# Performance work log

Hardware: AMD Instinct MI355X
Metric: run time of the kernel (lower is better)

The kernel has to match this reference:

```python
import jax, jax.numpy as jnp
import numpy as np

N = 20000      # num_nodes
H = 150        # hidden_channels
R = 35         # num_relations
B = 5          # num_blocks  -> block dims 30x30
E = 640000     # num_edges
IB = H // B


def _xavier(key, shape):
    fan_in, fan_out = shape[-2], shape[-1]
    lim = jnp.sqrt(6.0 / (fan_in + fan_out))
    return jax.random.uniform(key, shape, jnp.float32, -lim, lim)


def setup_inputs() -> dict:
    key = jax.random.key(0)
    ks = jax.random.split(key, 10)
    edge_index = jax.random.randint(ks[0], (2, E), 0, N, dtype=jnp.int64)
    edge_type = jax.random.randint(ks[1], (E,), 0, R, dtype=jnp.int64)
    return {
        "node_emb": _xavier(ks[2], (N, H)),
        "w1": _xavier(ks[3], (R, B, IB, IB)),      # relation block-diagonal weights
        "root1": _xavier(ks[4], (H, H)),
        "b1": jnp.zeros((H,), jnp.float32),
        "w2": _xavier(ks[5], (R, B, IB, IB)),
        "root2": _xavier(ks[6], (H, H)),
        "b2": jnp.zeros((H,), jnp.float32),
        "edge_index": edge_index,
        "edge_type": edge_type,
    }


def _rgcn_layer(x, w, root, bias, src, dst, etype):
    # PyG RGCNConv with num_blocks: per-relation block-diag transform of source
    # features, mean-aggregated per (dst, relation), summed over relations,
    # plus dense root transform and bias.
    # Linearity lets us aggregate (mean) FIRST, then transform: cheaper + exact.
    seg = dst * R + etype                                   # [E] segment per (node, rel)
    xs = x[src]                                             # [E, H] gather
    sums = jax.ops.segment_sum(xs, seg, num_segments=N * R)  # [N*R, H]
    cnt = jax.ops.segment_sum(jnp.ones((src.shape[0],), x.dtype), seg,
                              num_segments=N * R)           # [N*R]
    mean = sums / jnp.maximum(cnt, 1.0)[:, None]            # zero where no edges
    a = mean.reshape(N, R, B, IB)
    agg = jnp.einsum('nrbi,rbio->nbo', a, w).reshape(N, H)  # sum over relations
    return agg + x @ root + bias


def reference(node_emb, w1, root1, b1, w2, root2, b2, edge_index, edge_type):
    src, dst = edge_index[0], edge_index[1]
    x = _rgcn_layer(node_emb, w1, root1, b1, src, dst, edge_type)
    x = jax.nn.relu(x)
    # dropout p=0.2 is a no-op in eval mode
    x = _rgcn_layer(x, w2, root2, b2, src, dst, edge_type)
    return x
```

## Files before the change

kernel.cpp:

```cpp
#include <hip/hip_runtime.h>
#include <hip/hip_fp16.h>

#define H 150
#define RNUM 35
#define BNUM 5
#define IB 30

typedef unsigned short ushort_t;
typedef unsigned int uint_t;
using bf16x8 = __attribute__((ext_vector_type(8))) short;
using f32x4  = __attribute__((ext_vector_type(4))) float;

__device__ __forceinline__ ushort_t f2bf(float x) {
    union { float f; unsigned u; } v; v.f = x;
    unsigned u = v.u;
    return (ushort_t)((u + 0x7FFF + ((u >> 16) & 1)) >> 16);
}
__device__ __forceinline__ float bfLo(uint_t u) {
    union { unsigned u; float f; } v; v.u = u << 16; return v.f;
}
__device__ __forceinline__ float bfHi(uint_t u) {
    union { unsigned u; float f; } v; v.u = u & 0xffff0000u; return v.f;
}


__global__ void k_count(const int* __restrict__ ei, const int* __restrict__ et,
                        int E_, int* __restrict__ cnt) {
    for (int e = blockIdx.x * blockDim.x + threadIdx.x; e < E_; e += gridDim.x * blockDim.x) {
        int d = ei[E_ + e];
        int r = et[e];
        atomicAdd(&cnt[d * RNUM + r], 1);
    }
}

#define SPT 2
#define SCAN_BLOCK 256
#define SCAN_SPAN (SPT * SCAN_BLOCK)

__global__ void k_scanA(const int* __restrict__ cnt, int N_,
                        int* __restrict__ blkN, int* __restrict__ blkD) {
    __shared__ int sn[SCAN_BLOCK], sd[SCAN_BLOCK];
    int t = threadIdx.x;
    int base = blockIdx.x * SCAN_SPAN + t * SPT;
    int tn = 0, td = 0;
    for (int k = 0; k < SPT; ++k) {
        int d = base + k;
        if (d < N_) {
            for (int r = 0; r < RNUM; ++r) {
                int c = cnt[d * RNUM + r];
                if (c) { tn++; td += c; }
            }
        }
    }
    sn[t] = tn; sd[t] = td;
    __syncthreads();
    if (t == 0) {
        int an = 0, ad = 0;
        for (int i = 0; i < SCAN_BLOCK; ++i) { an += sn[i]; ad += sd[i]; }
        blkN[blockIdx.x] = an; blkD[blockIdx.x] = ad;
    }
}

__global__ void k_scanB(const int* __restrict__ blkN, const int* __restrict__ blkD,
                        int* __restrict__ blkBN, int* __restrict__ blkBD, int nblk) {
    if (threadIdx.x == 0 && blockIdx.x == 0) {
        int an = 0, ad = 0;
        for (int i = 0; i < nblk; ++i) {
            blkBN[i] = an; blkBD[i] = ad;
            an += blkN[i]; ad += blkD[i];
        }
    }
}

__global__ void k_scanC(const int* __restrict__ cnt, int N_,
                        const int* __restrict__ blkBN, const int* __restrict__ blkBD,
                        int* __restrict__ dstbase, int* __restrict__ segoff,
                        int* __restrict__ segidx, int* __restrict__ relhist2) {
    __shared__ int sn[SCAN_BLOCK], sd[SCAN_BLOCK];
    __shared__ int lhist[RNUM];
    int t = threadIdx.x;
    for (int i = t; i < RNUM; i += SCAN_BLOCK) lhist[i] = 0;
    int base = blockIdx.x * SCAN_SPAN + t * SPT;
    int tn = 0, td = 0;
    for (int k = 0; k < SPT; ++k) {
        int d = base + k;
        if (d < N_) {
            for (int r = 0; r < RNUM; ++r) {
                int c = cnt[d * RNUM + r];
                if (c) { tn++; td += c; }
            }
        }
    }
    sn[t] = tn; sd[t] = td;
    __syncthreads();
    if (t == 0) {
        int an = blkBN[blockIdx.x], ad = blkBD[blockIdx.x];
        for (int i = 0; i < SCAN_BLOCK; ++i) {
            int a = sn[i], b = sd[i];
            sn[i] = an; sd[i] = ad;
            an += a; ad += b;
        }
    }
    __syncthreads();
    int sb = sn[t], eb = sd[t];
    for (int k = 0; k < SPT; ++k) {
        int d = base + k;
        if (d < N_) {
            dstbase[d] = sb;
            for (int r = 0; r < RNUM; ++r) {
                int cell = d * RNUM + r;
                int c = cnt[cell];
                segoff[cell] = eb;
                if (c) { segidx[cell] = sb; sb++; eb += c; atomicAdd(&lhist[r], 1); }
            }
            if (d == N_ - 1) dstbase[N_] = sb;
        }
    }
    __syncthreads();
    for (int i = t; i < RNUM; i += SCAN_BLOCK)
        if (lhist[i]) atomicAdd(&relhist2[i], lhist[i]);
}

__global__ void k_relbase(const int* __restrict__ relhist2, int* __restrict__ relbase2,
                          int* __restrict__ tprefix) {
    if (threadIdx.x == 0 && blockIdx.x == 0) {
        int a = 0, tp = 0;
        for (int r = 0; r < RNUM; ++r) {
            relbase2[r] = a; tprefix[r] = tp;
            a += relhist2[r];
            tp += (relhist2[r] + 15) >> 4;
        }
        relbase2[RNUM] = a; tprefix[RNUM] = tp;
    }
}

__global__ void k_scatter2(const int* __restrict__ ei, const int* __restrict__ et,
                           int E_, int* __restrict__ segoff, int* __restrict__ ssrc2) {
    int e = blockIdx.x * blockDim.x + threadIdx.x;
    if (e >= E_) return;
    int r = et[e];
    int d = ei[E_ + e];
    int pos = atomicAdd(&segoff[d * RNUM + r], 1);
    ssrc2[pos] = ei[e];
}

__global__ void k_relassign(const int* __restrict__ cnt, const int* __restrict__ segoff,
                            const int* __restrict__ segidx, int Ncells,
                            const int* __restrict__ relbase2, int* __restrict__ relfill2,
                            int4* __restrict__ rec) {
    __shared__ int lh[RNUM];
    __shared__ int lbase[RNUM];
    for (int i = threadIdx.x; i < RNUM; i += blockDim.x) lh[i] = 0;
    __syncthreads();
    const int stride = gridDim.x * blockDim.x;
    for (int cell = blockIdx.x * blockDim.x + threadIdx.x; cell < Ncells; cell += stride)
        if (cnt[cell]) atomicAdd(&lh[cell % RNUM], 1);
    __syncthreads();
    for (int i = threadIdx.x; i < RNUM; i += blockDim.x) {
        int c = lh[i];
        lbase[i] = relbase2[i] + (c ? atomicAdd(&relfill2[i], c) : 0);
        lh[i] = 0;
    }
    __syncthreads();
    for (int cell = blockIdx.x * blockDim.x + threadIdx.x; cell < Ncells; cell += stride) {
        int c = cnt[cell];
        if (c) {
            int r = cell % RNUM;
            int pos = lbase[r] + atomicAdd(&lh[r], 1);
            rec[pos] = make_int4(segidx[cell], segoff[cell] - c, c, 0);
        }
    }
}

__global__ void k_prepw(const float* __restrict__ w1, const float* __restrict__ w2,
                        ushort_t* __restrict__ wb1, ushort_t* __restrict__ wb2) {
    const int tot = RNUM * BNUM * 2 * 16 * 32;
    int idx = blockIdx.x * blockDim.x + threadIdx.x;
    if (idx >= 2 * tot) return;
    const float* w = (idx < tot) ? w1 : w2;
    ushort_t* wb = (idx < tot) ? wb1 : wb2;
    int q = (idx < tot) ? idx : idx - tot;
    int kj = q & 7;
    int kg = (q >> 3) & 3;
    int cl = (q >> 5) & 15;
    int nh = (q >> 9) & 1;
    int rb = q >> 10;
    int k = kg * 8 + kj;
    int col = nh * 16 + cl;
    ushort_t v = 0;
    if (k < IB && col < IB) v = f2bf(w[(rb * IB + k) * IB + col]);
    wb[q] = v;
}

__global__ void k_convA(const float* __restrict__ x, ushort_t* __restrict__ xbf, int N_) {
    int i = blockIdx.x * blockDim.x + threadIdx.x;
    if (i >= N_ * 160) return;
    int n = i / 160, c = i - n * 160;
    xbf[i] = (c < H) ? f2bf(x[n * H + c]) : 0;
}

__global__ void k_convB(const float* __restrict__ r1, const float* __restrict__ r2,
                        ushort_t* __restrict__ B1, ushort_t* __restrict__ B2) {
    int i = blockIdx.x * blockDim.x + threadIdx.x;
    if (i >= 2 * 160 * 160) return;
    const float* src = (i < 160 * 160) ? r1 : r2;
    ushort_t* dst = (i < 160 * 160) ? B1 : B2;
    int k = (i < 160 * 160) ? i : i - 160 * 160;
    int row = k / 160, col = k - row * 160;
    dst[k] = (row < H && col < H) ? f2bf(src[row * H + col]) : 0;
}

__global__ __launch_bounds__(256) void k_rootmm(const ushort_t* __restrict__ Abf,
                                                const ushort_t* __restrict__ Bbf,
                                                const float* __restrict__ bias,
                                                float* __restrict__ Cout, int N_) {
    int nt = blockIdx.y;
    int wv = threadIdx.x >> 6, l = threadIdx.x & 63;
    int lr = l & 15, lk = l >> 4;
    bf16x8 bfr[5];
    #pragma unroll
    for (int ks = 0; ks < 5; ++ks) {
        #pragma unroll
        for (int j = 0; j < 8; ++j)
            bfr[ks][j] = (short)Bbf[(ks * 32 + lk * 8 + j) * 160 + nt * 16 + lr];
    }
    int mtiles = N_ / 16;
    int col = nt * 16 + lr;
    float bv = (col < H) ? bias[col] : 0.f;
    for (int mt = blockIdx.x * 4 + wv; mt < mtiles; mt += gridDim.x * 4) {
        f32x4 acc = {0.f, 0.f, 0.f, 0.f};
        const ushort_t* arow = Abf + (size_t)(mt * 16 + lr) * 160 + lk * 8;
        #pragma unroll
        for (int ks = 0; ks < 5; ++ks) {
            bf16x8 af = *reinterpret_cast<const bf16x8*>(arow + ks * 32);
            acc = __builtin_amdgcn_mfma_f32_16x16x32_bf16(af, bfr[ks], acc, 0, 0, 0);
        }
        if (col < H) {
            #pragma unroll
            for (int reg = 0; reg < 4; ++reg)
                Cout[(size_t)(mt * 16 + lk * 4 + reg) * H + col] = acc[reg] + bv;
        }
    }
}


#define ASTRIDE 168

__global__ __launch_bounds__(256, 4)
void k_seg(const int4* __restrict__ rec, const int* __restrict__ relbase2,
           const int* __restrict__ tprefix,
           const int* __restrict__ ssrc2, const ushort_t* __restrict__ wbf,
           const ushort_t* __restrict__ xbf, __half* __restrict__ tseg,
           const int* __restrict__ rowLoP, const int* __restrict__ rowHiP) {
    __shared__ ushort_t Abuf[4][16 * ASTRIDE];
    __shared__ int relb[RNUM + 1], tpre[RNUM + 1];
    int t = threadIdx.x, wv = t >> 6, l = t & 63;
    int lr = l & 15, kg = l >> 4;
    if (t < RNUM + 1) { relb[t] = relbase2[t]; tpre[t] = tprefix[t]; }
    __syncthreads();
    int rowLo = rowLoP[0], rowHi = rowHiP[0];
    int ntile_tot = tpre[RNUM];

    {
        uint_t* az = reinterpret_cast<uint_t*>(&Abuf[wv][0]);
        for (int i = l; i < 16 * ASTRIDE / 2; i += 64) az[i] = 0;
    }

    int i0 = 2 * l;
    int uA = (i0 / 30) * 16 + (i0 % 30) / 2 ? 0 : 0;
    uA = ((i0 / 30) * 32 + (i0 % 30)) >> 1;
    int i1 = 128 + 2 * l;
    int uB = ((i1 / 30) * 32 + (i1 % 30)) >> 1;

    for (int ti = blockIdx.x * 4 + wv; ti < ntile_tot; ti += gridDim.x * 4) {
        int r_lo = 0, r_hi = RNUM;
        while (r_hi - r_lo > 1) {
            int m = (r_lo + r_hi) >> 1;
            if (tpre[m] <= ti) r_lo = m; else r_hi = m;
        }
        int r = r_lo;
        int base = relb[r];
        int nseg = relb[r + 1] - base;
        int sbeg = (ti - tpre[r]) << 4;

        bf16x8 bfr[BNUM][2];
        #pragma unroll
        for (int b = 0; b < BNUM; ++b)
            #pragma unroll
            for (int nh = 0; nh < 2; ++nh)
                bfr[b][nh] = *reinterpret_cast<const bf16x8*>(
                    wbf + ((size_t)((r * BNUM + b) * 2 + nh) * 512) + lr * 32 + kg * 8);

        int4 myrec = make_int4(0x7fffffff, 0, 1, 0);
        if (l < 16 && sbeg + l < nseg) myrec = rec[base + sbeg + l];

        uint_t* Au = reinterpret_cast<uint_t*>(&Abuf[wv][0]);
        for (int s = 0; s < 16; ++s) {
            int row = __builtin_amdgcn_readfirstlane(__shfl(myrec.x, s));
            if (row < rowLo || row >= rowHi) continue;
            int eo = __builtin_amdgcn_readfirstlane(__shfl(myrec.y, s));
            int c  = __builtin_amdgcn_readfirstlane(__shfl(myrec.z, s));
            float a0 = 0.f, a1 = 0.f, a2 = 0.f, a3 = 0.f;
            for (int k = 0; k < c; ++k) {
                int src = ssrc2[eo + k];
                const uint_t* rowU = reinterpret_cast<const uint_t*>(xbf + (size_t)src * 160);
                uint_t u0 = rowU[l];
                a0 += bfLo(u0); a1 += bfHi(u0);
                if (l < 11) {
                    uint_t u1 = rowU[64 + l];
                    a2 += bfLo(u1); a3 += bfHi(u1);
                }
            }
            float inv = 1.0f / (float)c;
            uint_t p0 = (uint_t)f2bf(a0 * inv) | ((uint_t)f2bf(a1 * inv) << 16);
            Au[s * 84 + uA] = p0;
            if (l < 11) {
                uint_t p1 = (uint_t)f2bf(a2 * inv) | ((uint_t)f2bf(a3 * inv) << 16);
                Au[s * 84 + uB] = p1;
            }
        }

        int rg[4]; bool rok[4];
        #pragma unroll
        for (int q = 0; q < 4; ++q) {
            rg[q] = __shfl(myrec.x, kg * 4 + q);
            rok[q] = (rg[q] >= rowLo) && (rg[q] < rowHi);
        }

        #pragma unroll
        for (int b = 0; b < BNUM; ++b) {
            bf16x8 af = *reinterpret_cast<const bf16x8*>(
                &Abuf[wv][lr * ASTRIDE + b * 32 + kg * 8]);
            f32x4 acc0 = {0.f, 0.f, 0.f, 0.f};
            f32x4 acc1 = {0.f, 0.f, 0.f, 0.f};
            acc0 = __builtin_amdgcn_mfma_f32_16x16x32_bf16(af, bfr[b][0], acc0, 0, 0, 0);
            acc1 = __builtin_amdgcn_mfma_f32_16x16x32_bf16(af, bfr[b][1], acc1, 0, 0, 0);
            #pragma unroll
            for (int q = 0; q < 4; ++q) {
                if (rok[q]) {
                    __half* orow = tseg + (size_t)(rg[q] - rowLo) * H + b * IB;
                    orow[lr] = __float2half(acc0[q]);
                    if (lr < 14) orow[16 + lr] = __float2half(acc1[q]);
                }
            }
        }
    }
}


__global__ __launch_bounds__(256)
void k_aggadd(const __half* __restrict__ tseg, const int* __restrict__ dstbase,
              const float* __restrict__ rootsrc, float* __restrict__ fout,
              ushort_t* __restrict__ Abf, int relu, int s0, int s1) {
    int t = threadIdx.x, wv = t >> 6, l = t & 63;
    int segBase = dstbase[s0];
    for (int d = s0 + blockIdx.x * 4 + wv; d < s1; d += gridDim.x * 4) {
        int a = dstbase[d], bnd = dstbase[d + 1];
        const float* brow = rootsrc + (size_t)d * H;
        float2 acc0 = *reinterpret_cast<const float2*>(brow + 2 * l);
        float2 acc1 = make_float2(0.f, 0.f);
        if (l < 11) acc1 = *reinterpret_cast<const float2*>(brow + 128 + 2 * l);
        for (int s = a; s < bnd; ++s) {
            const __half2* trow = reinterpret_cast<const __half2*>(
                tseg + (size_t)(s - segBase) * H);
            float2 v = __half22float2(trow[l]);
            acc0.x += v.x; acc0.y += v.y;
            if (l < 11) {
                float2 v1 = __half22float2(trow[64 + l]);
                acc1.x += v1.x; acc1.y += v1.y;
            }
        }
        if (relu) {
            acc0.x = fmaxf(acc0.x, 0.f); acc0.y = fmaxf(acc0.y, 0.f);
            acc1.x = fmaxf(acc1.x, 0.f); acc1.y = fmaxf(acc1.y, 0.f);
        }
        if (fout) {
            float* frow = fout + (size_t)d * H;
            *reinterpret_cast<float2*>(frow + 2 * l) = acc0;
            if (l < 11) *reinterpret_cast<float2*>(frow + 128 + 2 * l) = acc1;
        }
        if (Abf) {
            ushort_t* arow = Abf + (size_t)d * 160;
            uint_t p0 = (uint_t)f2bf(acc0.x) | ((uint_t)f2bf(acc0.y) << 16);
            *reinterpret_cast<uint_t*>(arow + 2 * l) = p0;
            if (l < 11) {
                uint_t p1 = (uint_t)f2bf(acc1.x) | ((uint_t)f2bf(acc1.y) << 16);
                *reinterpret_cast<uint_t*>(arow + 128 + 2 * l) = p1;
            }
            if (l < 5) *reinterpret_cast<uint_t*>(arow + 150 + 2 * l) = 0;
        }
    }
}

extern "C" void kernel_launch(void* const* d_in, const int* in_sizes, int n_in,
                              void* d_out, int out_size, void* d_ws, size_t ws_size,
                              hipStream_t stream) {
    const float* node_emb = (const float*)d_in[0];
    const float* w1 = (const float*)d_in[1];
    const float* root1 = (const float*)d_in[2];
    const float* b1 = (const float*)d_in[3];
    const float* w2 = (const float*)d_in[4];
    const float* root2 = (const float*)d_in[5];
    const float* b2 = (const float*)d_in[6];
    const int* edge_index = (const int*)d_in[7];
    const int* edge_type = (const int*)d_in[8];
    int N_ = in_sizes[0] / H;
    int E_ = in_sizes[8];
    float* out = (float*)d_out;

    const int Ncells = N_ * RNUM;
    const int wbtot = RNUM * BNUM * 2 * 16 * 32;

    int* ws = (int*)d_ws;
    size_t off = 0;
    int* cnt      = ws + off; off += Ncells;
    int* relhist2 = ws + off; off += 64;
    int* relfill2 = ws + off; off += 64;
    size_t zero_units = off;
    int* relbase2 = ws + off; off += 64;
    int* tprefix  = ws + off; off += 64;
    int* blkN     = ws + off; off += 64;
    int* blkD     = ws + off; off += 64;
    int* blkBN    = ws + off; off += 64;
    int* blkBD    = ws + off; off += 64;
    int* dstbase  = ws + off; off += N_ + 2;
    int* segoff   = ws + off; off += Ncells;
    int* segidx   = ws + off; off += Ncells;
    int* ssrc2    = ws + off; off += E_;
    off = (off + 3) & ~(size_t)3;
    int4* rec     = (int4*)(ws + off); off += (size_t)4 * Ncells;
    ushort_t* wbf1 = (ushort_t*)(ws + off); off += wbtot / 2;
    ushort_t* wbf2 = (ushort_t*)(ws + off); off += wbtot / 2;
    ushort_t* Bbf1 = (ushort_t*)(ws + off); off += 12800;
    ushort_t* Bbf2 = (ushort_t*)(ws + off); off += 12800;
    ushort_t* xbf  = (ushort_t*)(ws + off); off += (size_t)N_ * 160 / 2;
    ushort_t* Abf  = (ushort_t*)(ws + off); off += (size_t)N_ * 160 / 2;
    float* rootbuf = (float*)(ws + off); off += (size_t)N_ * H;
    __half* tseg  = (__half*)(ws + off);
    size_t tsegOffB = off * 4;

    size_t availB = (ws_size > tsegOffB) ? (ws_size - tsegOffB) : 0;
    long long dps_ll = (long long)(availB / ((size_t)RNUM * H * 2));
    int dps = (dps_ll > N_) ? N_ : (int)dps_ll;
    if (dps < 1) dps = 1;
    int nstripe = (N_ + dps - 1) / dps;

    hipMemsetAsync(cnt, 0, zero_units * 4, stream);

    k_count<<<512, 256, 0, stream>>>(edge_index, edge_type, E_, cnt);
    int nscan = (N_ + SCAN_SPAN - 1) / SCAN_SPAN;
    k_scanA<<<nscan, SCAN_BLOCK, 0, stream>>>(cnt, N_, blkN, blkD);
    k_scanB<<<1, 64, 0, stream>>>(blkN, blkD, blkBN, blkBD, nscan);
    k_scanC<<<nscan, SCAN_BLOCK, 0, stream>>>(cnt, N_, blkBN, blkBD, dstbase, segoff,
                                              segidx, relhist2);
    k_relbase<<<1, 64, 0, stream>>>(relhist2, relbase2, tprefix);
    k_scatter2<<<(E_ + 255) / 256, 256, 0, stream>>>(edge_index, edge_type, E_, segoff, ssrc2);
    k_relassign<<<64, 256, 0, stream>>>(cnt, segoff, segidx, Ncells, relbase2, relfill2, rec);
    k_prepw<<<(2 * wbtot + 255) / 256, 256, 0, stream>>>(w1, w2, wbf1, wbf2);
    k_convB<<<(2 * 160 * 160 + 255) / 256, 256, 0, stream>>>(root1, root2, Bbf1, Bbf2);
    k_convA<<<(N_ * 160 + 255) / 256, 256, 0, stream>>>(node_emb, xbf, N_);

    const int SEG_GRID = 1792;

    k_rootmm<<<dim3(40, 10), 256, 0, stream>>>(xbf, Bbf1, b1, rootbuf, N_);
    for (int st = 0; st < nstripe; ++st) {
        int s0 = st * dps;
        int s1 = s0 + dps; if (s1 > N_) s1 = N_;
        k_seg<<<SEG_GRID, 256, 0, stream>>>(rec, relbase2, tprefix, ssrc2, wbf1, xbf, tseg,
                                            dstbase + s0, dstbase + s1);
        k_aggadd<<<1280, 256, 0, stream>>>(tseg, dstbase, rootbuf, (float*)nullptr, Abf,
                                           1, s0, s1);
    }

    k_rootmm<<<dim3(40, 10), 256, 0, stream>>>(Abf, Bbf2, b2, out, N_);
    for (int st = 0; st < nstripe; ++st) {
        int s0 = st * dps;
        int s1 = s0 + dps; if (s1 > N_) s1 = N_;
        k_seg<<<SEG_GRID, 256, 0, stream>>>(rec, relbase2, tprefix, ssrc2, wbf2, Abf, tseg,
                                            dstbase + s0, dstbase + s1);
        k_aggadd<<<1280, 256, 0, stream>>>(tseg, dstbase, out, out, (ushort_t*)nullptr,
                                           0, s0, s1);
    }
}
```

Before: 455.5 us.

## Store per-segment transforms in relation-sorted order with LDS-staged coalesced writes

k_seg now writes its transformed segment rows into tseg in the relation-sorted record order, indexed by record position. The rows are first staged in LDS so each wave can write them out with contiguous 16-byte stores instead of scattered half-precision stores. k_aggadd uses a new inverse map from segment to record to gather these rows, and it accumulates in place into the output across stripes. Stripes now split the record index range instead of the destination range, and the record struct shrinks from int4 to int2, which cuts the memory traffic in k_seg at the cost of an extra indirect lookup in aggregation.

```diff
diff --git a/kernel.cpp b/kernel.cpp
--- a/kernel.cpp
+++ b/kernel.cpp
@@ -147,7 +147,7 @@
 __global__ void k_relassign(const int* __restrict__ cnt, const int* __restrict__ segoff,
                             const int* __restrict__ segidx, int Ncells,
                             const int* __restrict__ relbase2, int* __restrict__ relfill2,
-                            int4* __restrict__ rec) {
+                            int2* __restrict__ rec, int* __restrict__ inv) {
     __shared__ int lh[RNUM];
     __shared__ int lbase[RNUM];
     for (int i = threadIdx.x; i < RNUM; i += blockDim.x) lh[i] = 0;
@@ -167,7 +167,8 @@
         if (c) {
             int r = cell % RNUM;
             int pos = lbase[r] + atomicAdd(&lh[r], 1);
-            rec[pos] = make_int4(segidx[cell], segoff[cell] - c, c, 0);
+            rec[pos] = make_int2(segoff[cell] - c, c);
+            inv[segidx[cell]] = pos;
         }
     }
 }
@@ -245,30 +246,29 @@
 
 
 #define ASTRIDE 168
+#define TSTRIDE 152
 
 __global__ __launch_bounds__(256, 4)
-void k_seg(const int4* __restrict__ rec, const int* __restrict__ relbase2,
+void k_seg(const int2* __restrict__ rec, const int* __restrict__ relbase2,
            const int* __restrict__ tprefix,
            const int* __restrict__ ssrc2, const ushort_t* __restrict__ wbf,
-           const ushort_t* __restrict__ xbf, __half* __restrict__ tseg,
-           const int* __restrict__ rowLoP, const int* __restrict__ rowHiP) {
+           const ushort_t* __restrict__ xbf, ushort_t* __restrict__ tseg,
+           int rmLo, int rmHi) {
     __shared__ ushort_t Abuf[4][16 * ASTRIDE];
     __shared__ int relb[RNUM + 1], tpre[RNUM + 1];
     int t = threadIdx.x, wv = t >> 6, l = t & 63;
     int lr = l & 15, kg = l >> 4;
     if (t < RNUM + 1) { relb[t] = relbase2[t]; tpre[t] = tprefix[t]; }
-    __syncthreads();
-    int rowLo = rowLoP[0], rowHi = rowHiP[0];
-    int ntile_tot = tpre[RNUM];
 
     {
         uint_t* az = reinterpret_cast<uint_t*>(&Abuf[wv][0]);
         for (int i = l; i < 16 * ASTRIDE / 2; i += 64) az[i] = 0;
     }
+    __syncthreads();
+    int ntile_tot = tpre[RNUM];
 
     int i0 = 2 * l;
-    int uA = (i0 / 30) * 16 + (i0 % 30) / 2 ? 0 : 0;
-    uA = ((i0 / 30) * 32 + (i0 % 30)) >> 1;
+    int uA = ((i0 / 30) * 32 + (i0 % 30)) >> 1;
     int i1 = 128 + 2 * l;
     int uB = ((i1 / 30) * 32 + (i1 % 30)) >> 1;
 
@@ -282,6 +282,11 @@
         int base = relb[r];
         int nseg = relb[r + 1] - base;
         int sbeg = (ti - tpre[r]) << 4;
+        int gr0 = base + sbeg;
+        int valid = nseg - sbeg; if (valid > 16) valid = 16;
+        int r0 = rmLo - gr0; if (r0 < 0) r0 = 0;
+        int r1 = rmHi - gr0; if (r1 > valid) r1 = valid;
+        if (r1 <= r0) continue;
 
         bf16x8 bfr[BNUM][2];
         #pragma unroll
@@ -291,15 +296,13 @@
                 bfr[b][nh] = *reinterpret_cast<const bf16x8*>(
                     wbf + ((size_t)((r * BNUM + b) * 2 + nh) * 512) + lr * 32 + kg * 8);
 
-        int4 myrec = make_int4(0x7fffffff, 0, 1, 0);
+        int2 myrec = make_int2(0, 1);
         if (l < 16 && sbeg + l < nseg) myrec = rec[base + sbeg + l];
 
         uint_t* Au = reinterpret_cast<uint_t*>(&Abuf[wv][0]);
-        for (int s = 0; s < 16; ++s) {
-            int row = __builtin_amdgcn_readfirstlane(__shfl(myrec.x, s));
-            if (row < rowLo || row >= rowHi) continue;
-            int eo = __builtin_amdgcn_readfirstlane(__shfl(myrec.y, s));
-            int c  = __builtin_amdgcn_readfirstlane(__shfl(myrec.z, s));
+        for (int s = r0; s < r1; ++s) {
+            int eo = __builtin_amdgcn_readfirstlane(__shfl(myrec.x, s));
+            int c  = __builtin_amdgcn_readfirstlane(__shfl(myrec.y, s));
             float a0 = 0.f, a1 = 0.f, a2 = 0.f, a3 = 0.f;
             for (int k = 0; k < c; ++k) {
                 int src = ssrc2[eo + k];
@@ -320,49 +323,59 @@
             }
         }
 
-        int rg[4]; bool rok[4];
-        #pragma unroll
-        for (int q = 0; q < 4; ++q) {
-            rg[q] = __shfl(myrec.x, kg * 4 + q);
-            rok[q] = (rg[q] >= rowLo) && (rg[q] < rowHi);
-        }
-
+        f32x4 acc0[BNUM], acc1[BNUM];
         #pragma unroll
         for (int b = 0; b < BNUM; ++b) {
             bf16x8 af = *reinterpret_cast<const bf16x8*>(
                 &Abuf[wv][lr * ASTRIDE + b * 32 + kg * 8]);
-            f32x4 acc0 = {0.f, 0.f, 0.f, 0.f};
-            f32x4 acc1 = {0.f, 0.f, 0.f, 0.f};
-            acc0 = __builtin_amdgcn_mfma_f32_16x16x32_bf16(af, bfr[b][0], acc0, 0, 0, 0);
-            acc1 = __builtin_amdgcn_mfma_f32_16x16x32_bf16(af, bfr[b][1], acc1, 0, 0, 0);
+            f32x4 z = {0.f, 0.f, 0.f, 0.f};
+            acc0[b] = __builtin_amdgcn_mfma_f32_16x16x32_bf16(af, bfr[b][0], z, 0, 0, 0);
+            acc1[b] = __builtin_amdgcn_mfma_f32_16x16x32_bf16(af, bfr[b][1], z, 0, 0, 0);
+        }
+        asm volatile("" ::: "memory");
+
+        ushort_t* stg = &Abuf[wv][0];
+        #pragma unroll
+        for (int q = 0; q < 4; ++q) {
+            int row = kg * 4 + q;
             #pragma unroll
-            for (int q = 0; q < 4; ++q) {
-                if (rok[q]) {
-                    __half* orow = tseg + (size_t)(rg[q] - rowLo) * H + b * IB;
-                    orow[lr] = __float2half(acc0[q]);
-                    if (lr < 14) orow[16 + lr] = __float2half(acc1[q]);
-                }
-            }
+            for (int b = 0; b < BNUM; ++b) {
+                stg[row * TSTRIDE + b * IB + lr] = __half_as_ushort(__float2half(acc0[b][q]));
+                if (lr < 14)
+                    stg[row * TSTRIDE + b * IB + 16 + lr] = __half_as_ushort(__float2half(acc1[b][q]));
+            }
+        }
+        asm volatile("" ::: "memory");
+
+        {
+            int ndw4 = (r1 - r0) * (TSTRIDE / 8);
+            const uint4* lsrc = reinterpret_cast<const uint4*>(stg + r0 * TSTRIDE);
+            uint4* gdst = reinterpret_cast<uint4*>(
+                tseg + (size_t)(gr0 + r0 - rmLo) * TSTRIDE);
+            for (int i = l; i < ndw4; i += 64)
+                gdst[i] = lsrc[i];
         }
     }
 }
 
 
 __global__ __launch_bounds__(256)
-void k_aggadd(const __half* __restrict__ tseg, const int* __restrict__ dstbase,
-              const float* __restrict__ rootsrc, float* __restrict__ fout,
-              ushort_t* __restrict__ Abf, int relu, int s0, int s1) {
+void k_aggadd(const ushort_t* __restrict__ tseg, const int* __restrict__ dstbase,
+              const int* __restrict__ inv, float* __restrict__ fout,
+              ushort_t* __restrict__ Abf, int relu, int finalize,
+              int rmLo, int rmHi, int N_) {
     int t = threadIdx.x, wv = t >> 6, l = t & 63;
-    int segBase = dstbase[s0];
-    for (int d = s0 + blockIdx.x * 4 + wv; d < s1; d += gridDim.x * 4) {
+    for (int d = blockIdx.x * 4 + wv; d < N_; d += gridDim.x * 4) {
         int a = dstbase[d], bnd = dstbase[d + 1];
-        const float* brow = rootsrc + (size_t)d * H;
-        float2 acc0 = *reinterpret_cast<const float2*>(brow + 2 * l);
+        float* frow = fout + (size_t)d * H;
+        float2 acc0 = *reinterpret_cast<const float2*>(frow + 2 * l);
         float2 acc1 = make_float2(0.f, 0.f);
-        if (l < 11) acc1 = *reinterpret_cast<const float2*>(brow + 128 + 2 * l);
+        if (l < 11) acc1 = *reinterpret_cast<const float2*>(frow + 128 + 2 * l);
         for (int s = a; s < bnd; ++s) {
+            int row = inv[s];
+            if (row < rmLo || row >= rmHi) continue;
             const __half2* trow = reinterpret_cast<const __half2*>(
-                tseg + (size_t)(s - segBase) * H);
+                tseg + (size_t)(row - rmLo) * TSTRIDE);
             float2 v = __half22float2(trow[l]);
             acc0.x += v.x; acc0.y += v.y;
             if (l < 11) {
@@ -370,16 +383,13 @@
                 acc1.x += v1.x; acc1.y += v1.y;
             }
         }
-        if (relu) {
+        if (finalize && relu) {
             acc0.x = fmaxf(acc0.x, 0.f); acc0.y = fmaxf(acc0.y, 0.f);
             acc1.x = fmaxf(acc1.x, 0.f); acc1.y = fmaxf(acc1.y, 0.f);
         }
-        if (fout) {
-            float* frow = fout + (size_t)d * H;
-            *reinterpret_cast<float2*>(frow + 2 * l) = acc0;
-            if (l < 11) *reinterpret_cast<float2*>(frow + 128 + 2 * l) = acc1;
-        }
-        if (Abf) {
+        *reinterpret_cast<float2*>(frow + 2 * l) = acc0;
+        if (l < 11) *reinterpret_cast<float2*>(frow + 128 + 2 * l) = acc1;
+        if (finalize && Abf) {
             ushort_t* arow = Abf + (size_t)d * 160;
             uint_t p0 = (uint_t)f2bf(acc0.x) | ((uint_t)f2bf(acc0.y) << 16);
             *reinterpret_cast<uint_t*>(arow + 2 * l) = p0;
@@ -426,9 +436,10 @@
     int* dstbase  = ws + off; off += N_ + 2;
     int* segoff   = ws + off; off += Ncells;
     int* segidx   = ws + off; off += Ncells;
+    int* inv      = ws + off; off += Ncells;
     int* ssrc2    = ws + off; off += E_;
     off = (off + 3) & ~(size_t)3;
-    int4* rec     = (int4*)(ws + off); off += (size_t)4 * Ncells;
+    int2* rec     = (int2*)(ws + off); off += (size_t)2 * Ncells;
     ushort_t* wbf1 = (ushort_t*)(ws + off); off += wbtot / 2;
     ushort_t* wbf2 = (ushort_t*)(ws + off); off += wbtot / 2;
     ushort_t* Bbf1 = (ushort_t*)(ws + off); off += 12800;
@@ -436,14 +447,15 @@
     ushort_t* xbf  = (ushort_t*)(ws + off); off += (size_t)N_ * 160 / 2;
     ushort_t* Abf  = (ushort_t*)(ws + off); off += (size_t)N_ * 160 / 2;
     float* rootbuf = (float*)(ws + off); off += (size_t)N_ * H;
-    __half* tseg  = (__half*)(ws + off);
+    ushort_t* tseg = (ushort_t*)(ws + off);
     size_t tsegOffB = off * 4;
 
     size_t availB = (ws_size > tsegOffB) ? (ws_size - tsegOffB) : 0;
-    long long dps_ll = (long long)(availB / ((size_t)RNUM * H * 2));
-    int dps = (dps_ll > N_) ? N_ : (int)dps_ll;
-    if (dps < 1) dps = 1;
-    int nstripe = (N_ + dps - 1) / dps;
+    int maxRows = (E_ < Ncells) ? E_ : Ncells;
+    long long rps_ll = (long long)(availB / (TSTRIDE * 2));
+    int rps = (rps_ll > maxRows) ? maxRows : (int)rps_ll;
+    if (rps < 1) rps = 1;
+    int nstripe = (maxRows + rps - 1) / rps;
 
     hipMemsetAsync(cnt, 0, zero_units * 4, stream);
 
@@ -455,7 +467,8 @@
                                               segidx, relhist2);
     k_relbase<<<1, 64, 0, stream>>>(relhist2, relbase2, tprefix);
     k_scatter2<<<(E_ + 255) / 256, 256, 0, stream>>>(edge_index, edge_type, E_, segoff, ssrc2);
-    k_relassign<<<64, 256, 0, stream>>>(cnt, segoff, segidx, Ncells, relbase2, relfill2, rec);
+    k_relassign<<<64, 256, 0, stream>>>(cnt, segoff, segidx, Ncells, relbase2, relfill2,
+                                        rec, inv);
     k_prepw<<<(2 * wbtot + 255) / 256, 256, 0, stream>>>(w1, w2, wbf1, wbf2);
     k_convB<<<(2 * 160 * 160 + 255) / 256, 256, 0, stream>>>(root1, root2, Bbf1, Bbf2);
     k_convA<<<(N_ * 160 + 255) / 256, 256, 0, stream>>>(node_emb, xbf, N_);
@@ -464,21 +477,23 @@
 
     k_rootmm<<<dim3(40, 10), 256, 0, stream>>>(xbf, Bbf1, b1, rootbuf, N_);
     for (int st = 0; st < nstripe; ++st) {
-        int s0 = st * dps;
-        int s1 = s0 + dps; if (s1 > N_) s1 = N_;
-        k_seg<<<SEG_GRID, 256, 0, stream>>>(rec, relbase2, tprefix, ssrc2, wbf1, xbf, tseg,
-                                            dstbase + s0, dstbase + s1);
-        k_aggadd<<<1280, 256, 0, stream>>>(tseg, dstbase, rootbuf, (float*)nullptr, Abf,
-                                           1, s0, s1);
+        int rmLo = st * rps;
+        int rmHi = rmLo + rps; if (rmHi > maxRows) rmHi = maxRows;
+        int fin = (st == nstripe - 1);
+        k_seg<<<SEG_GRID, 256, 0, stream>>>(rec, relbase2, tprefix, ssrc2, wbf1, xbf,
+                                            tseg, rmLo, rmHi);
+        k_aggadd<<<1280, 256, 0, stream>>>(tseg, dstbase, inv, rootbuf, Abf, 1, fin,
+                                           rmLo, rmHi, N_);
     }
 
     k_rootmm<<<dim3(40, 10), 256, 0, stream>>>(Abf, Bbf2, b2, out, N_);
     for (int st = 0; st < nstripe; ++st) {
-        int s0 = st * dps;
-        int s1 = s0 + dps; if (s1 > N_) s1 = N_;
-        k_seg<<<SEG_GRID, 256, 0, stream>>>(rec, relbase2, tprefix, ssrc2, wbf2, Abf, tseg,
-                                            dstbase + s0, dstbase + s1);
-        k_aggadd<<<1280, 256, 0, stream>>>(tseg, dstbase, out, out, (ushort_t*)nullptr,
-                                           0, s0, s1);
-    }
-}
+        int rmLo = st * rps;
+        int rmHi = rmLo + rps; if (rmHi > maxRows) rmHi = maxRows;
+        int fin = (st == nstripe - 1);
+        k_seg<<<SEG_GRID, 256, 0, stream>>>(rec, relbase2, tprefix, ssrc2, wbf2, Abf,
+                                            tseg, rmLo, rmHi);
+        k_aggadd<<<1280, 256, 0, stream>>>(tseg, dstbase, inv, out, (ushort_t*)nullptr,
+                                           0, fin, rmLo, rmHi, N_);
+    }
+}
```

Measured after the change: 579.9 us. 1.27x slower.

## Split segment gather into per-block feature pools with separate node-feature copies

Applied to the files above, without the earlier changes.

Node features are stored as three extra bf16 arrays, one per group of diagonal blocks (blocks 0-1, 2-3, 4), and k_seg blocks are assigned by blockIdx to one pool. Each pool only gathers its own slice of columns and runs the MFMAs for its blocks. Several segments are now processed per wave in parallel, and ssrc and tseg use nontemporal load/store. The intent is a smaller per-pool working set for better cache locality and fewer idle lanes in the gather. The cost is extra memory for the duplicated feature layouts, and each tile's records and binary search are repeated across the three pools.

```diff
diff --git a/kernel.cpp b/kernel.cpp
--- a/kernel.cpp
+++ b/kernel.cpp
@@ -192,11 +192,20 @@
     wb[q] = v;
 }
 
-__global__ void k_convA(const float* __restrict__ x, ushort_t* __restrict__ xbf, int N_) {
+__global__ void k_convA(const float* __restrict__ x, uint_t* __restrict__ xbf,
+                        uint_t* __restrict__ xA, uint_t* __restrict__ xB,
+                        uint_t* __restrict__ xC, int N_) {
     int i = blockIdx.x * blockDim.x + threadIdx.x;
-    if (i >= N_ * 160) return;
-    int n = i / 160, c = i - n * 160;
-    xbf[i] = (c < H) ? f2bf(x[n * H + c]) : 0;
+    if (i >= N_ * 80) return;
+    int n = i / 80, j = i - n * 80;
+    uint_t u = 0;
+    if (j < 75) {
+        u = (uint_t)f2bf(x[n * H + 2 * j]) | ((uint_t)f2bf(x[n * H + 2 * j + 1]) << 16);
+        if (j < 30) xA[(size_t)n * 32 + j] = u;
+        else if (j < 60) xB[(size_t)n * 32 + (j - 30)] = u;
+        else xC[(size_t)n * 16 + (j - 60)] = u;
+    }
+    xbf[(size_t)n * 80 + j] = u;
 }
 
 __global__ void k_convB(const float* __restrict__ r1, const float* __restrict__ r2,
@@ -248,31 +257,44 @@
 
 __global__ __launch_bounds__(256, 4)
 void k_seg(const int4* __restrict__ rec, const int* __restrict__ relbase2,
-           const int* __restrict__ tprefix,
-           const int* __restrict__ ssrc2, const ushort_t* __restrict__ wbf,
-           const ushort_t* __restrict__ xbf, __half* __restrict__ tseg,
+           const int* __restrict__ tprefix, const int* __restrict__ ssrc2,
+           const ushort_t* __restrict__ wbf,
+           const uint_t* __restrict__ xA, const uint_t* __restrict__ xB,
+           const uint_t* __restrict__ xC, ushort_t* __restrict__ tseg,
            const int* __restrict__ rowLoP, const int* __restrict__ rowHiP) {
     __shared__ ushort_t Abuf[4][16 * ASTRIDE];
     __shared__ int relb[RNUM + 1], tpre[RNUM + 1];
     int t = threadIdx.x, wv = t >> 6, l = t & 63;
     int lr = l & 15, kg = l >> 4;
     if (t < RNUM + 1) { relb[t] = relbase2[t]; tpre[t] = tprefix[t]; }
-    __syncthreads();
-    int rowLo = rowLoP[0], rowHi = rowHiP[0];
-    int ntile_tot = tpre[RNUM];
-
     {
         uint_t* az = reinterpret_cast<uint_t*>(&Abuf[wv][0]);
         for (int i = l; i < 16 * ASTRIDE / 2; i += 64) az[i] = 0;
     }
-
-    int i0 = 2 * l;
-    int uA = (i0 / 30) * 16 + (i0 % 30) / 2 ? 0 : 0;
-    uA = ((i0 / 30) * 32 + (i0 % 30)) >> 1;
-    int i1 = 128 + 2 * l;
-    int uB = ((i1 / 30) * 32 + (i1 % 30)) >> 1;
-
-    for (int ti = blockIdx.x * 4 + wv; ti < ntile_tot; ti += gridDim.x * 4) {
+    __syncthreads();
+    int rowLo = rowLoP[0], rowHi = rowHiP[0];
+    int ntile_tot = tpre[RNUM];
+
+    int role = blockIdx.x & 7;
+    int pool, pidx, poolBlocks, bLo, bCnt;
+    if (role < 3)      { pool = 0; pidx = (blockIdx.x >> 3) * 3 + role;       poolBlocks = (gridDim.x >> 3) * 3; bLo = 0; bCnt = 2; }
+    else if (role < 6) { pool = 1; pidx = (blockIdx.x >> 3) * 3 + (role - 3); poolBlocks = (gridDim.x >> 3) * 3; bLo = 2; bCnt = 2; }
+    else               { pool = 2; pidx = (blockIdx.x >> 3) * 2 + (role - 6); poolBlocks = (gridDim.x >> 3) * 2; bLo = 4; bCnt = 1; }
+    const uint_t* xs = (pool == 0) ? xA : (pool == 1) ? xB : xC;
+    int xstride = (pool == 2) ? 16 : 32;
+    int lpsh = (pool == 2) ? 4 : 5;
+    int li = l & ((1 << lpsh) - 1);
+    int sg = l >> lpsh;
+    int nsp = 64 >> lpsh;
+    int nact = (pool == 2) ? 15 : 30;
+    bool lact = li < nact;
+    int blk = (2 * li) / 30;
+    int uoff = (bLo + blk) * 16 + (li - blk * 15);
+
+    int slot = pidx * 4 + wv;
+    int tstride = poolBlocks * 4;
+
+    for (int ti = slot; ti < ntile_tot; ti += tstride) {
         int r_lo = 0, r_hi = RNUM;
         while (r_hi - r_lo > 1) {
             int m = (r_lo + r_hi) >> 1;
@@ -282,41 +304,38 @@
         int base = relb[r];
         int nseg = relb[r + 1] - base;
         int sbeg = (ti - tpre[r]) << 4;
-
-        bf16x8 bfr[BNUM][2];
+        int valid = nseg - sbeg; if (valid > 16) valid = 16;
+
+        bf16x8 bfr[2][2];
         #pragma unroll
-        for (int b = 0; b < BNUM; ++b)
-            #pragma unroll
-            for (int nh = 0; nh < 2; ++nh)
-                bfr[b][nh] = *reinterpret_cast<const bf16x8*>(
-                    wbf + ((size_t)((r * BNUM + b) * 2 + nh) * 512) + lr * 32 + kg * 8);
+        for (int bi = 0; bi < 2; ++bi) {
+            if (bi < bCnt) {
+                #pragma unroll
+                for (int nh = 0; nh < 2; ++nh)
+                    bfr[bi][nh] = *reinterpret_cast<const bf16x8*>(
+                        wbf + ((size_t)((r * BNUM + bLo + bi) * 2 + nh) * 512) + lr * 32 + kg * 8);
+            }
+        }
 
         int4 myrec = make_int4(0x7fffffff, 0, 1, 0);
-        if (l < 16 && sbeg + l < nseg) myrec = rec[base + sbeg + l];
+        if (l < 16 && l < valid) myrec = rec[base + sbeg + l];
 
         uint_t* Au = reinterpret_cast<uint_t*>(&Abuf[wv][0]);
-        for (int s = 0; s < 16; ++s) {
-            int row = __builtin_amdgcn_readfirstlane(__shfl(myrec.x, s));
-            if (row < rowLo || row >= rowHi) continue;
-            int eo = __builtin_amdgcn_readfirstlane(__shfl(myrec.y, s));
-            int c  = __builtin_amdgcn_readfirstlane(__shfl(myrec.z, s));
-            float a0 = 0.f, a1 = 0.f, a2 = 0.f, a3 = 0.f;
-            for (int k = 0; k < c; ++k) {
-                int src = ssrc2[eo + k];
-                const uint_t* rowU = reinterpret_cast<const uint_t*>(xbf + (size_t)src * 160);
-                uint_t u0 = rowU[l];
-                a0 += bfLo(u0); a1 += bfHi(u0);
-                if (l < 11) {
-                    uint_t u1 = rowU[64 + l];
-                    a2 += bfLo(u1); a3 += bfHi(u1);
+        for (int s0 = 0; s0 < valid; s0 += nsp) {
+            int sA = s0 + sg;
+            int rowA = __shfl(myrec.x, sA);
+            int eo   = __shfl(myrec.y, sA);
+            int c    = __shfl(myrec.z, sA);
+            bool ok = lact && (sA < valid) && (rowA >= rowLo) && (rowA < rowHi);
+            if (ok) {
+                float a0 = 0.f, a1 = 0.f;
+                for (int k = 0; k < c; ++k) {
+                    int src = __builtin_nontemporal_load(&ssrc2[eo + k]);
+                    uint_t u = xs[(size_t)src * xstride + li];
+                    a0 += bfLo(u); a1 += bfHi(u);
                 }
-            }
-            float inv = 1.0f / (float)c;
-            uint_t p0 = (uint_t)f2bf(a0 * inv) | ((uint_t)f2bf(a1 * inv) << 16);
-            Au[s * 84 + uA] = p0;
-            if (l < 11) {
-                uint_t p1 = (uint_t)f2bf(a2 * inv) | ((uint_t)f2bf(a3 * inv) << 16);
-                Au[s * 84 + uB] = p1;
+                float inv = 1.0f / (float)c;
+                Au[sA * 84 + uoff] = (uint_t)f2bf(a0 * inv) | ((uint_t)f2bf(a1 * inv) << 16);
             }
         }
 
@@ -328,19 +347,21 @@
         }
 
         #pragma unroll
-        for (int b = 0; b < BNUM; ++b) {
+        for (int bi = 0; bi < 2; ++bi) {
+            if (bi >= bCnt) continue;
+            int b = bLo + bi;
             bf16x8 af = *reinterpret_cast<const bf16x8*>(
                 &Abuf[wv][lr * ASTRIDE + b * 32 + kg * 8]);
-            f32x4 acc0 = {0.f, 0.f, 0.f, 0.f};
-            f32x4 acc1 = {0.f, 0.f, 0.f, 0.f};
-            acc0 = __builtin_amdgcn_mfma_f32_16x16x32_bf16(af, bfr[b][0], acc0, 0, 0, 0);
-            acc1 = __builtin_amdgcn_mfma_f32_16x16x32_bf16(af, bfr[b][1], acc1, 0, 0, 0);
+            f32x4 z = {0.f, 0.f, 0.f, 0.f};
+            f32x4 acc0 = __builtin_amdgcn_mfma_f32_16x16x32_bf16(af, bfr[bi][0], z, 0, 0, 0);
+            f32x4 acc1 = __builtin_amdgcn_mfma_f32_16x16x32_bf16(af, bfr[bi][1], z, 0, 0, 0);
             #pragma unroll
             for (int q = 0; q < 4; ++q) {
                 if (rok[q]) {
-                    __half* orow = tseg + (size_t)(rg[q] - rowLo) * H + b * IB;
-                    orow[lr] = __float2half(acc0[q]);
-                    if (lr < 14) orow[16 + lr] = __float2half(acc1[q]);
+                    ushort_t* orow = tseg + (size_t)(rg[q] - rowLo) * H + b * IB;
+                    __builtin_nontemporal_store(__half_as_ushort(__float2half(acc0[q])), orow + lr);
+                    if (lr < 14)
+                        __builtin_nontemporal_store(__half_as_ushort(__float2half(acc1[q])), orow + 16 + lr);
                 }
             }
         }
@@ -349,14 +370,15 @@
 
 
 __global__ __launch_bounds__(256)
-void k_aggadd(const __half* __restrict__ tseg, const int* __restrict__ dstbase,
-              const float* __restrict__ rootsrc, float* __restrict__ fout,
-              ushort_t* __restrict__ Abf, int relu, int s0, int s1) {
+void k_aggadd(const ushort_t* __restrict__ tseg, const int* __restrict__ dstbase,
+              float* __restrict__ buf, uint_t* __restrict__ Abf,
+              uint_t* __restrict__ aA, uint_t* __restrict__ aB, uint_t* __restrict__ aC,
+              int relu, int s0, int s1) {
     int t = threadIdx.x, wv = t >> 6, l = t & 63;
     int segBase = dstbase[s0];
     for (int d = s0 + blockIdx.x * 4 + wv; d < s1; d += gridDim.x * 4) {
         int a = dstbase[d], bnd = dstbase[d + 1];
-        const float* brow = rootsrc + (size_t)d * H;
+        float* brow = buf + (size_t)d * H;
         float2 acc0 = *reinterpret_cast<const float2*>(brow + 2 * l);
         float2 acc1 = make_float2(0.f, 0.f);
         if (l < 11) acc1 = *reinterpret_cast<const float2*>(brow + 128 + 2 * l);
@@ -374,20 +396,18 @@
             acc0.x = fmaxf(acc0.x, 0.f); acc0.y = fmaxf(acc0.y, 0.f);
             acc1.x = fmaxf(acc1.x, 0.f); acc1.y = fmaxf(acc1.y, 0.f);
         }
-        if (fout) {
-            float* frow = fout + (size_t)d * H;
-            *reinterpret_cast<float2*>(frow + 2 * l) = acc0;
-            if (l < 11) *reinterpret_cast<float2*>(frow + 128 + 2 * l) = acc1;
-        }
+        *reinterpret_cast<float2*>(brow + 2 * l) = acc0;
+        if (l < 11) *reinterpret_cast<float2*>(brow + 128 + 2 * l) = acc1;
         if (Abf) {
-            ushort_t* arow = Abf + (size_t)d * 160;
             uint_t p0 = (uint_t)f2bf(acc0.x) | ((uint_t)f2bf(acc0.y) << 16);
-            *reinterpret_cast<uint_t*>(arow + 2 * l) = p0;
-            if (l < 11) {
-                uint_t p1 = (uint_t)f2bf(acc1.x) | ((uint_t)f2bf(acc1.y) << 16);
-                *reinterpret_cast<uint_t*>(arow + 128 + 2 * l) = p1;
-            }
-            if (l < 5) *reinterpret_cast<uint_t*>(arow + 150 + 2 * l) = 0;
+            uint_t p1 = (uint_t)f2bf(acc1.x) | ((uint_t)f2bf(acc1.y) << 16);
+            Abf[(size_t)d * 80 + l] = p0;
+            if (l < 11) Abf[(size_t)d * 80 + 64 + l] = p1;
+            if (l < 5)  Abf[(size_t)d * 80 + 75 + l] = 0;
+            if (l < 30) aA[(size_t)d * 32 + l] = p0;
+            else if (l < 60) aB[(size_t)d * 32 + (l - 30)] = p0;
+            else aC[(size_t)d * 16 + (l - 60)] = p0;
+            if (l < 11) aC[(size_t)d * 16 + 4 + l] = p1;
         }
     }
 }
@@ -433,10 +453,16 @@
     ushort_t* wbf2 = (ushort_t*)(ws + off); off += wbtot / 2;
     ushort_t* Bbf1 = (ushort_t*)(ws + off); off += 12800;
     ushort_t* Bbf2 = (ushort_t*)(ws + off); off += 12800;
-    ushort_t* xbf  = (ushort_t*)(ws + off); off += (size_t)N_ * 160 / 2;
-    ushort_t* Abf  = (ushort_t*)(ws + off); off += (size_t)N_ * 160 / 2;
+    uint_t* xbf  = (uint_t*)(ws + off); off += (size_t)N_ * 80;
+    uint_t* Abf  = (uint_t*)(ws + off); off += (size_t)N_ * 80;
+    uint_t* xA   = (uint_t*)(ws + off); off += (size_t)N_ * 32;
+    uint_t* xB   = (uint_t*)(ws + off); off += (size_t)N_ * 32;
+    uint_t* xC   = (uint_t*)(ws + off); off += (size_t)N_ * 16;
+    uint_t* aA   = (uint_t*)(ws + off); off += (size_t)N_ * 32;
+    uint_t* aB   = (uint_t*)(ws + off); off += (size_t)N_ * 32;
+    uint_t* aC   = (uint_t*)(ws + off); off += (size_t)N_ * 16;
     float* rootbuf = (float*)(ws + off); off += (size_t)N_ * H;
-    __half* tseg  = (__half*)(ws + off);
+    ushort_t* tseg = (ushort_t*)(ws + off);
     size_t tsegOffB = off * 4;
 
     size_t availB = (ws_size > tsegOffB) ? (ws_size - tsegOffB) : 0;
@@ -458,27 +484,28 @@
     k_relassign<<<64, 256, 0, stream>>>(cnt, segoff, segidx, Ncells, relbase2, relfill2, rec);
     k_prepw<<<(2 * wbtot + 255) / 256, 256, 0, stream>>>(w1, w2, wbf1, wbf2);
     k_convB<<<(2 * 160 * 160 + 255) / 256, 256, 0, stream>>>(root1, root2, Bbf1, Bbf2);
-    k_convA<<<(N_ * 160 + 255) / 256, 256, 0, stream>>>(node_emb, xbf, N_);
+    k_convA<<<(N_ * 80 + 255) / 256, 256, 0, stream>>>(node_emb, xbf, xA, xB, xC, N_);
 
     const int SEG_GRID = 1792;
 
-    k_rootmm<<<dim3(40, 10), 256, 0, stream>>>(xbf, Bbf1, b1, rootbuf, N_);
+    k_rootmm<<<dim3(40, 10), 256, 0, stream>>>((const ushort_t*)xbf, Bbf1, b1, rootbuf, N_);
     for (int st = 0; st < nstripe; ++st) {
         int s0 = st * dps;
         int s1 = s0 + dps; if (s1 > N_) s1 = N_;
-        k_seg<<<SEG_GRID, 256, 0, stream>>>(rec, relbase2, tprefix, ssrc2, wbf1, xbf, tseg,
-                                            dstbase + s0, dstbase + s1);
-        k_aggadd<<<1280, 256, 0, stream>>>(tseg, dstbase, rootbuf, (float*)nullptr, Abf,
+        k_seg<<<SEG_GRID, 256, 0, stream>>>(rec, relbase2, tprefix, ssrc2, wbf1,
+                                            xA, xB, xC, tseg, dstbase + s0, dstbase + s1);
+        k_aggadd<<<1280, 256, 0, stream>>>(tseg, dstbase, rootbuf, Abf, aA, aB, aC,
                                            1, s0, s1);
     }
 
-    k_rootmm<<<dim3(40, 10), 256, 0, stream>>>(Abf, Bbf2, b2, out, N_);
+    k_rootmm<<<dim3(40, 10), 256, 0, stream>>>((const ushort_t*)Abf, Bbf2, b2, out, N_);
     for (int st = 0; st < nstripe; ++st) {
         int s0 = st * dps;
         int s1 = s0 + dps; if (s1 > N_) s1 = N_;
-        k_seg<<<SEG_GRID, 256, 0, stream>>>(rec, relbase2, tprefix, ssrc2, wbf2, Abf, tseg,
-                                            dstbase + s0, dstbase + s1);
-        k_aggadd<<<1280, 256, 0, stream>>>(tseg, dstbase, out, out, (ushort_t*)nullptr,
+        k_seg<<<SEG_GRID, 256, 0, stream>>>(rec, relbase2, tprefix, ssrc2, wbf2,
+                                            aA, aB, aC, tseg, dstbase + s0, dstbase + s1);
+        k_aggadd<<<1280, 256, 0, stream>>>(tseg, dstbase, out, (uint_t*)nullptr,
+                                           (uint_t*)nullptr, (uint_t*)nullptr, (uint_t*)nullptr,
                                            0, s0, s1);
     }
 }
```

After: 854.6 us. +87.6%, slower.
